# Kernel optimization log

Hardware: AMD Instinct MI355X
Metric: run time of the kernel (lower is better)

Reference implementation:

```python
import jax, jax.numpy as jnp
import numpy as np

B, S, E, H = 4, 4096, 256, 2048
EPS = 1e-5

def layernorm(x, g, b):
    mu = jnp.mean(x, axis=-1, keepdims=True)
    var = jnp.mean(jnp.square(x - mu), axis=-1, keepdims=True)
    return (x - mu) * jax.lax.rsqrt(var + EPS) * g + b

def setup_inputs() -> dict:
    key = jax.random.key(0)
    ks = jax.random.split(key, 16)
    sE = 1.0 / np.sqrt(E)
    sH = 1.0 / np.sqrt(H)
    return {
        "x_embeddings": jax.random.normal(ks[0], (B, S, E), dtype=jnp.float32),
        "wq": jax.random.normal(ks[1], (E, E), dtype=jnp.float32) * sE,
        "bq": jnp.zeros((E,), jnp.float32),
        "wk": jax.random.normal(ks[2], (E, E), dtype=jnp.float32) * sE,
        "bk": jnp.zeros((E,), jnp.float32),
        "wv": jax.random.normal(ks[3], (E, E), dtype=jnp.float32) * sE,
        "bv": jnp.zeros((E,), jnp.float32),
        "w0": jax.random.normal(ks[4], (E, E), dtype=jnp.float32) * sE,
        "b0": jnp.zeros((E,), jnp.float32),
        "w1": jax.random.normal(ks[5], (E, H), dtype=jnp.float32) * sE,
        "b1": jnp.zeros((H,), jnp.float32),
        "ln_mlp_g": jnp.ones((H,), jnp.float32),
        "ln_mlp_b": jnp.zeros((H,), jnp.float32),
        "w2": jax.random.normal(ks[6], (H, E), dtype=jnp.float32) * sH,
        "b2": jnp.zeros((E,), jnp.float32),
        "ln1_g": jnp.ones((E,), jnp.float32),
        "ln1_b": jnp.zeros((E,), jnp.float32),
        "ln2_g": jnp.ones((E,), jnp.float32),
        "ln2_b": jnp.zeros((E,), jnp.float32),
    }

def reference(x_embeddings, wq, bq, wk, bk, wv, bv, w0, b0,
              w1, b1, ln_mlp_g, ln_mlp_b, w2, b2,
              ln1_g, ln1_b, ln2_g, ln2_b):
    x = x_embeddings
    q = x @ wq + bq
    k = x @ wk + bk
    v = x @ wv + bv
    # Unscaled, unmasked attention (faithful to source: no 1/sqrt(d), mask unused)
    scores = jnp.einsum('bqd,bkd->bqk', q, k)          # [B,S,S]
    probs = jax.nn.softmax(scores, axis=-1)
    attn = jnp.einsum('bqk,bkd->bqd', probs, v)        # [B,S,E]
    e = layernorm(x + attn, ln1_g, ln1_b) @ w0 + b0
    h = e @ w1 + b1                                     # [B,S,H]
    h = jax.nn.leaky_relu(layernorm(h, ln_mlp_g, ln_mlp_b))  # LnActivation: LN + LeakyReLU
    logits = h @ w2 + b2                                # [B,S,E]
    return layernorm(jax.nn.leaky_relu(logits + e), ln2_g, ln2_b)
```

## Files before the change

### kernel.cpp

```cpp
#include <hip/hip_runtime.h>

typedef unsigned short u16;
typedef unsigned int   u32;
typedef u16   u16x4 __attribute__((ext_vector_type(4)));
typedef u16   u16x8 __attribute__((ext_vector_type(8)));
typedef short s16x8 __attribute__((ext_vector_type(8)));
typedef float f32x4 __attribute__((ext_vector_type(4)));
typedef _Float16 f16x8 __attribute__((ext_vector_type(8)));

__device__ __forceinline__ u16 f2b(float f) {
  u32 u = __builtin_bit_cast(u32, f);
  u32 r = (u + 0x7fffu + ((u >> 16) & 1u)) >> 16;
  return (u16)r;
}
__device__ __forceinline__ float b2f(u16 h) {
  return __builtin_bit_cast(float, (u32)h << 16);
}
__device__ __forceinline__ u16 f2h(float f) {
  _Float16 h = (_Float16)f;
  return __builtin_bit_cast(u16, h);
}

__device__ __forceinline__ void async16(void* l, const void* g) {
  __builtin_amdgcn_global_load_lds((const __attribute__((address_space(1))) u32*)g,
                                   (__attribute__((address_space(3))) u32*)l, 16, 0, 0);
}

__device__ __forceinline__ float wave_sum(float v) {
#pragma unroll
  for (int m = 32; m; m >>= 1) v += __shfl_xor(v, m, 64);
  return v;
}

constexpr int BM = 128, BN = 128, BK = 64;

template<bool SPLIT, int OMODE>
__global__ __launch_bounds__(256)
void k_gemm_bt(const u16* __restrict__ Ah, const u16* __restrict__ Al, long lda,
               const u16* __restrict__ Bh, const u16* __restrict__ Bl, long ldb,
               const float* __restrict__ bias,
               float* __restrict__ Cf, u16* __restrict__ Cb, u16* __restrict__ Cl,
               long ldc, int K)
{
  __shared__ u16 lds[(SPLIT ? 4 : 2) * BM * BK];
  const int tid = threadIdx.x;
  const long arow0 = (long)blockIdx.y * BM;
  const long bcol0 = (long)blockIdx.x * BN;

  long offA[4], offB[4];
#pragma unroll
  for (int r = 0; r < 4; ++r) {
    const int off = r * 4096 + tid * 16;
    const int row = off >> 7;
    const int colb = off & 127;
    offA[r] = (arow0 + row) * lda + (colb >> 1);
    offB[r] = (bcol0 + row) * ldb + (colb >> 1);
  }

  const int lane = tid & 63;
  const int wid = tid >> 6;
  const int wr = (wid >> 1) * 64;
  const int wc = (wid & 1) * 64;
  const int fr = lane & 15;
  const int fk = (lane >> 4) * 8;

  f32x4 acc[4][4] = {};

  for (int k0 = 0; k0 < K; k0 += BK) {
#pragma unroll
    for (int r = 0; r < 4; ++r) {
      const int loff = (r * 4096 + tid * 16) >> 1;
      async16(&lds[loff],           Ah + offA[r] + k0);
      async16(&lds[BM*BK + loff],   Bh + offB[r] + k0);
      if constexpr (SPLIT) {
        async16(&lds[2*BM*BK + loff], Al + offA[r] + k0);
        async16(&lds[3*BM*BK + loff], Bl + offB[r] + k0);
      }
    }
    __syncthreads();
#pragma unroll
    for (int kk = 0; kk < BK; kk += 32) {
      s16x8 a[4], b[4];
#pragma unroll
      for (int m = 0; m < 4; ++m)
        a[m] = *(const s16x8*)&lds[(wr + m*16 + fr) * BK + kk + fk];
#pragma unroll
      for (int n = 0; n < 4; ++n)
        b[n] = *(const s16x8*)&lds[BM*BK + (wc + n*16 + fr) * BK + kk + fk];
#pragma unroll
      for (int m = 0; m < 4; ++m)
#pragma unroll
        for (int n = 0; n < 4; ++n)
          acc[m][n] = __builtin_amdgcn_mfma_f32_16x16x32_bf16(a[m], b[n], acc[m][n], 0, 0, 0);
      if constexpr (SPLIT) {
        s16x8 al[4], bl[4];
#pragma unroll
        for (int m = 0; m < 4; ++m)
          al[m] = *(const s16x8*)&lds[2*BM*BK + (wr + m*16 + fr) * BK + kk + fk];
#pragma unroll
        for (int n = 0; n < 4; ++n)
          bl[n] = *(const s16x8*)&lds[3*BM*BK + (wc + n*16 + fr) * BK + kk + fk];
#pragma unroll
        for (int m = 0; m < 4; ++m)
#pragma unroll
          for (int n = 0; n < 4; ++n) {
            acc[m][n] = __builtin_amdgcn_mfma_f32_16x16x32_bf16(a[m], bl[n], acc[m][n], 0, 0, 0);
            acc[m][n] = __builtin_amdgcn_mfma_f32_16x16x32_bf16(al[m], b[n], acc[m][n], 0, 0, 0);
          }
      }
    }
    __syncthreads();
  }

  float bv[4];
#pragma unroll
  for (int n = 0; n < 4; ++n) {
    const long gcol = bcol0 + wc + n*16 + fr;
    bv[n] = bias ? bias[gcol] : 0.f;
  }

#pragma unroll
  for (int m = 0; m < 4; ++m) {
#pragma unroll
    for (int reg = 0; reg < 4; ++reg) {
      const long grow = arow0 + wr + m*16 + (lane >> 4) * 4 + reg;
      const long ro = grow * ldc;
#pragma unroll
      for (int n = 0; n < 4; ++n) {
        const long gcol = bcol0 + wc + n*16 + fr;
        const float val = acc[m][n][reg] + bv[n];
        if constexpr (OMODE == 0) {
          Cf[ro + gcol] = val;
        } else if constexpr (OMODE == 1) {
          Cb[ro + gcol] = f2b(val);
        } else if constexpr (OMODE == 4) {
          Cb[ro + gcol] = f2h(val);
        } else {
          const u16 hb = f2b(val);
          Cb[ro + gcol] = hb;
          Cl[ro + gcol] = f2b(val - b2f(hb));
        }
      }
    }
  }
}

__global__ __launch_bounds__(256)
void k_flash(const u16* __restrict__ q16, const u16* __restrict__ k16,
             const u16* __restrict__ vt,
             u16* __restrict__ attn)
{
  __shared__ u16 lkh[2][32*256];
  __shared__ float lS[32*36];
  __shared__ u16 lP[32*40];
  __shared__ float lm[32], ll[32], lsc[32];

  const int tid = threadIdx.x;
  const int lane = tid & 63, wid = tid >> 6;
  const long bo = (long)blockIdx.y * 1048576;
  const long q0 = (long)blockIdx.x * 32;

  const int fr  = lane & 15;
  const int hi2 = lane >> 4;
  const int fk  = hi2 * 8;
  const int qh_sel = wid >> 1;
  const int kh_sel = wid & 1;

  f16x8 qf[8];
  {
    const u16* qp = q16 + bo + (q0 + qh_sel*16 + fr) * 256;
#pragma unroll
    for (int c = 0; c < 8; ++c)
      qf[c] = *(const f16x8*)(qp + c*32 + fk);
  }

  if (tid < 32) { lm[tid] = -1e30f; ll[tid] = 0.f; }
  f32x4 acc[2][4] = {};

  const char* kp = (const char*)(k16 + bo);
  const u16* vbase = vt + bo;

  auto STAGE = [&](int k0s, int b) {
#pragma unroll
    for (int r = 0; r < 4; ++r) {
      const int L = r*4096 + tid*16;
      const int row = L >> 9;
      const int colb = L & 511;
      const long gb = (long)(k0s + row)*512 + (colb ^ ((row & 7) << 4));
      async16((char*)lkh[b] + L, kp + gb);
    }
  };

  STAGE(0, 0);
  __syncthreads();

  int cur = 0;
  for (int k0 = 0; k0 < 4096; k0 += 32) {
    s16x8 vb[4];
#pragma unroll
    for (int j = 0; j < 4; ++j)
      vb[j] = *(const s16x8*)(vbase + (long)(wid*64 + j*16 + fr)*4096 + k0 + fk);

    if (k0 + 32 < 4096) STAGE(k0 + 32, cur ^ 1);

    f32x4 s0 = {};
    const int kc = kh_sel*16 + fr;
    const int swz = (kc & 7) << 4;
#pragma unroll
    for (int c = 0; c < 8; ++c) {
      const int o = (c*64 + hi2*16) ^ swz;
      const f16x8 bh = *(const f16x8*)((const char*)lkh[cur] + kc*512 + o);
      s0 = __builtin_amdgcn_mfma_f32_16x16x32_f16(qf[c], bh, s0, 0, 0, 0);
    }
#pragma unroll
    for (int r = 0; r < 4; ++r)
      lS[(qh_sel*16 + hi2*4 + r)*36 + kh_sel*16 + fr] = s0[r];
    __syncthreads();

    {
      const int sr = tid >> 3;
      const int sc = (tid & 7) * 4;
      const float4 sv = *(const float4*)&lS[sr*36 + sc];
      float tmx = fmaxf(fmaxf(sv.x, sv.y), fmaxf(sv.z, sv.w));
#pragma unroll
      for (int m = 1; m < 8; m <<= 1) tmx = fmaxf(tmx, __shfl_xor(tmx, m, 64));
      const float mold = lm[sr];
      const float mnew = fmaxf(mold, tmx);
      const float p0 = __expf(sv.x - mnew), p1 = __expf(sv.y - mnew);
      const float p2 = __expf(sv.z - mnew), p3 = __expf(sv.w - mnew);
      float ps = p0 + p1 + p2 + p3;
#pragma unroll
      for (int m = 1; m < 8; m <<= 1) ps += __shfl_xor(ps, m, 64);
      const float scale = __expf(mold - mnew);
      if ((tid & 7) == 0) {
        lm[sr] = mnew;
        ll[sr] = ll[sr] * scale + ps;
        lsc[sr] = scale;
      }
      u16x4 pb; pb[0]=f2b(p0); pb[1]=f2b(p1); pb[2]=f2b(p2); pb[3]=f2b(p3);
      *(u16x4*)&lP[sr*40 + sc] = pb;
    }
    __syncthreads();

#pragma unroll
    for (int qm = 0; qm < 2; ++qm)
#pragma unroll
      for (int r = 0; r < 4; ++r) {
        const float s = lsc[qm*16 + hi2*4 + r];
#pragma unroll
        for (int j = 0; j < 4; ++j) acc[qm][j][r] *= s;
      }
#pragma unroll
    for (int qm = 0; qm < 2; ++qm) {
      const s16x8 pa = *(const s16x8*)&lP[(qm*16 + fr)*40 + fk];
#pragma unroll
      for (int j = 0; j < 4; ++j)
        acc[qm][j] = __builtin_amdgcn_mfma_f32_16x16x32_bf16(pa, vb[j], acc[qm][j], 0, 0, 0);
    }
    cur ^= 1;
  }

  __syncthreads();
#pragma unroll
  for (int qm = 0; qm < 2; ++qm)
#pragma unroll
    for (int r = 0; r < 4; ++r) {
      const int row = qm*16 + hi2*4 + r;
      const float inv = 1.0f / ll[row];
      u16* op = attn + bo + (q0 + row)*256 + wid*64 + fr;
#pragma unroll
      for (int j = 0; j < 4; ++j)
        op[j*16] = f2b(acc[qm][j][r] * inv);
    }
}


__global__ __launch_bounds__(256)
void k_split_cast(const float* __restrict__ in, u16* __restrict__ hi, u16* __restrict__ lo, long n4) {
  long i = (long)blockIdx.x * 256 + threadIdx.x;
  if (i >= n4) return;
  float4 v = ((const float4*)in)[i];
  float vv[4] = {v.x, v.y, v.z, v.w};
  u16x4 h, l;
#pragma unroll
  for (int j = 0; j < 4; ++j) {
    u16 hb = f2b(vv[j]);
    h[j] = hb;
    l[j] = f2b(vv[j] - b2f(hb));
  }
  ((u16x4*)hi)[i] = h;
  ((u16x4*)lo)[i] = l;
}

template<bool SPLIT>
__global__ __launch_bounds__(256)
void k_transpose_f32(const float* __restrict__ in, u16* __restrict__ hi, u16* __restrict__ lo,
                     int R, int C) {
  __shared__ float t[32][33];
  const int c0 = blockIdx.x * 32, r0 = blockIdx.y * 32;
  const int tx = threadIdx.x, ty = threadIdx.y;
#pragma unroll
  for (int i = 0; i < 4; ++i)
    t[ty + i*8][tx] = in[(long)(r0 + ty + i*8) * C + c0 + tx];
  __syncthreads();
#pragma unroll
  for (int i = 0; i < 4; ++i) {
    const float f = t[tx][ty + i*8];
    const long o = (long)(c0 + ty + i*8) * R + r0 + tx;
    const u16 hb = f2b(f);
    hi[o] = hb;
    if constexpr (SPLIT) lo[o] = f2b(f - b2f(hb));
  }
}

__global__ __launch_bounds__(256)
void k_transpose_bf16(const u16* __restrict__ in, u16* __restrict__ out,
                      int R, int C, long sIn, long sOut) {
  __shared__ u16 t[32][34];
  const int z = blockIdx.z;
  const u16* ib = in + (long)z * sIn;
  u16* ob = out + (long)z * sOut;
  const int c0 = blockIdx.x * 32, r0 = blockIdx.y * 32;
  const int tx = threadIdx.x, ty = threadIdx.y;
#pragma unroll
  for (int i = 0; i < 4; ++i)
    t[ty + i*8][tx] = ib[(long)(r0 + ty + i*8) * C + c0 + tx];
  __syncthreads();
#pragma unroll
  for (int i = 0; i < 4; ++i)
    ob[(long)(c0 + ty + i*8) * R + r0 + tx] = t[tx][ty + i*8];
}

__global__ __launch_bounds__(256)
void k_add_ln(const float* __restrict__ x, const u16* __restrict__ a,
              const float* __restrict__ g, const float* __restrict__ b,
              u16* __restrict__ out) {
  const long row = (long)blockIdx.x * 4 + (threadIdx.x >> 6);
  const int lane = threadIdx.x & 63;
  const long base = row * 256 + lane * 4;
  const float4 xv = *(const float4*)(x + base);
  const u16x4 av = *(const u16x4*)(a + base);
  float t[4] = {xv.x + b2f(av[0]), xv.y + b2f(av[1]), xv.z + b2f(av[2]), xv.w + b2f(av[3])};
  float s = t[0] + t[1] + t[2] + t[3];
  float q = t[0]*t[0] + t[1]*t[1] + t[2]*t[2] + t[3]*t[3];
  s = wave_sum(s); q = wave_sum(q);
  const float mu = s * (1.f / 256.f);
  const float var = q * (1.f / 256.f) - mu * mu;
  const float rs = rsqrtf(var + 1e-5f);
  const float4 gv = *(const float4*)(g + lane * 4);
  const float4 bv = *(const float4*)(b + lane * 4);
  u16x4 o;
  o[0] = f2b((t[0] - mu) * rs * gv.x + bv.x);
  o[1] = f2b((t[1] - mu) * rs * gv.y + bv.y);
  o[2] = f2b((t[2] - mu) * rs * gv.z + bv.z);
  o[3] = f2b((t[3] - mu) * rs * gv.w + bv.w);
  *(u16x4*)(out + base) = o;
}

__global__ __launch_bounds__(256)
void k_ln_leaky(const u16* __restrict__ h, const float* __restrict__ g,
                const float* __restrict__ b, u16* __restrict__ out) {
  const long row = blockIdx.x;
  const int tid = threadIdx.x;
  const int lane = tid & 63, wid = tid >> 6;
  const u16x8 hv = *(const u16x8*)(h + row * 2048 + tid * 8);
  float f[8];
  float s = 0.f, q = 0.f;
#pragma unroll
  for (int j = 0; j < 8; ++j) { f[j] = b2f(hv[j]); s += f[j]; q += f[j] * f[j]; }
  s = wave_sum(s); q = wave_sum(q);
  __shared__ float rs_[4], rq_[4];
  if (lane == 0) { rs_[wid] = s; rq_[wid] = q; }
  __syncthreads();
  s = rs_[0] + rs_[1] + rs_[2] + rs_[3];
  q = rq_[0] + rq_[1] + rq_[2] + rq_[3];
  const float mu = s * (1.f / 2048.f);
  const float var = q * (1.f / 2048.f) - mu * mu;
  const float rsq = rsqrtf(var + 1e-5f);
  const float4 g0 = *(const float4*)(g + tid * 8);
  const float4 g1 = *(const float4*)(g + tid * 8 + 4);
  const float4 b0 = *(const float4*)(b + tid * 8);
  const float4 b1 = *(const float4*)(b + tid * 8 + 4);
  const float gg[8] = {g0.x, g0.y, g0.z, g0.w, g1.x, g1.y, g1.z, g1.w};
  const float bb[8] = {b0.x, b0.y, b0.z, b0.w, b1.x, b1.y, b1.z, b1.w};
  u16x8 o;
#pragma unroll
  for (int j = 0; j < 8; ++j) {
    float y = (f[j] - mu) * rsq * gg[j] + bb[j];
    y = y > 0.f ? y : 0.01f * y;
    o[j] = f2b(y);
  }
  *(u16x8*)(out + row * 2048 + tid * 8) = o;
}

__global__ __launch_bounds__(256)
void k_final(const float* __restrict__ lg, const u16* __restrict__ e,
             const float* __restrict__ g, const float* __restrict__ b,
             float* __restrict__ out) {
  const long row = (long)blockIdx.x * 4 + (threadIdx.x >> 6);
  const int lane = threadIdx.x & 63;
  const long base = row * 256 + lane * 4;
  const float4 lv = *(const float4*)(lg + base);
  const u16x4 ev = *(const u16x4*)(e + base);
  float t[4] = {lv.x + b2f(ev[0]), lv.y + b2f(ev[1]), lv.z + b2f(ev[2]), lv.w + b2f(ev[3])};
#pragma unroll
  for (int j = 0; j < 4; ++j) t[j] = t[j] > 0.f ? t[j] : 0.01f * t[j];
  float s = t[0] + t[1] + t[2] + t[3];
  float q = t[0]*t[0] + t[1]*t[1] + t[2]*t[2] + t[3]*t[3];
  s = wave_sum(s); q = wave_sum(q);
  const float mu = s * (1.f / 256.f);
  const float var = q * (1.f / 256.f) - mu * mu;
  const float rs = rsqrtf(var + 1e-5f);
  const float4 gv = *(const float4*)(g + lane * 4);
  const float4 bv = *(const float4*)(b + lane * 4);
  float4 o;
  o.x = (t[0] - mu) * rs * gv.x + bv.x;
  o.y = (t[1] - mu) * rs * gv.y + bv.y;
  o.z = (t[2] - mu) * rs * gv.z + bv.z;
  o.w = (t[3] - mu) * rs * gv.w + bv.w;
  *(float4*)(out + base) = o;
}


extern "C" void kernel_launch(void* const* d_in, const int* in_sizes, int n_in,
                              void* d_out, int out_size, void* d_ws, size_t ws_size,
                              hipStream_t stream) {
  const float* x   = (const float*)d_in[0];
  const float* wq  = (const float*)d_in[1];
  const float* bq  = (const float*)d_in[2];
  const float* wk  = (const float*)d_in[3];
  const float* bk  = (const float*)d_in[4];
  const float* wv  = (const float*)d_in[5];
  const float* bv_ = (const float*)d_in[6];
  const float* w0  = (const float*)d_in[7];
  const float* b0  = (const float*)d_in[8];
  const float* w1  = (const float*)d_in[9];
  const float* b1  = (const float*)d_in[10];
  const float* lmg = (const float*)d_in[11];
  const float* lmb = (const float*)d_in[12];
  const float* w2  = (const float*)d_in[13];
  const float* b2  = (const float*)d_in[14];
  const float* l1g = (const float*)d_in[15];
  const float* l1b = (const float*)d_in[16];
  const float* l2g = (const float*)d_in[17];
  const float* l2b = (const float*)d_in[18];

  char* ws = (char*)d_ws;
  float* out = (float*)d_out;

  u16* q16    = (u16*)(ws + 0);
  u16* k16    = (u16*)(ws + 16777216);
  u16* vT     = (u16*)(ws + 33554432);
  u16* x_hi   = (u16*)(ws + 41943040);
  u16* x_lo   = (u16*)(ws + 50331648);
  u16* v_b    = (u16*)(ws + 58720256);
  u16* attn_b = (u16*)(ws + 67108864);
  u16* ln1    = (u16*)(ws + 75497472);
  u16* e_b    = (u16*)(ws + 83886080);
  float* logits = (float*)(ws + 92274688);
  u16* h_b    = (u16*)(ws + 0);
  u16* wqT_h  = (u16*)(ws + 109051904);
  u16* wqT_l  = (u16*)(ws + 109182976);
  u16* wkT_h  = (u16*)(ws + 109314048);
  u16* wkT_l  = (u16*)(ws + 109445120);
  u16* wvT    = (u16*)(ws + 109576192);
  u16* w0T    = (u16*)(ws + 109707264);
  u16* w1T    = (u16*)(ws + 109838336);
  u16* w2T    = (u16*)(ws + 110886912);

  const dim3 t256(256);
  const dim3 tr(32, 8);

  k_split_cast<<<4096, t256, 0, stream>>>(x, x_hi, x_lo, 1048576);
  k_transpose_f32<true ><<<dim3(8, 8),  tr, 0, stream>>>(wq, wqT_h, wqT_l, 256, 256);
  k_transpose_f32<true ><<<dim3(8, 8),  tr, 0, stream>>>(wk, wkT_h, wkT_l, 256, 256);
  k_transpose_f32<false><<<dim3(8, 8),  tr, 0, stream>>>(wv, wvT, nullptr, 256, 256);
  k_transpose_f32<false><<<dim3(8, 8),  tr, 0, stream>>>(w0, w0T, nullptr, 256, 256);
  k_transpose_f32<false><<<dim3(64, 8), tr, 0, stream>>>(w1, w1T, nullptr, 256, 2048);
  k_transpose_f32<false><<<dim3(8, 64), tr, 0, stream>>>(w2, w2T, nullptr, 2048, 256);

  k_gemm_bt<true, 4><<<dim3(2, 128), t256, 0, stream>>>(
      x_hi, x_lo, 256, wqT_h, wqT_l, 256, bq, nullptr, q16, nullptr, 256, 256);
  k_gemm_bt<true, 4><<<dim3(2, 128), t256, 0, stream>>>(
      x_hi, x_lo, 256, wkT_h, wkT_l, 256, bk, nullptr, k16, nullptr, 256, 256);
  k_gemm_bt<false, 1><<<dim3(2, 128), t256, 0, stream>>>(
      x_hi, nullptr, 256, wvT, nullptr, 256, bv_, nullptr, v_b, nullptr, 256, 256);
  k_transpose_bf16<<<dim3(8, 128, 4), tr, 0, stream>>>(v_b, vT, 4096, 256, 1048576, 1048576);

  k_flash<<<dim3(128, 4), t256, 0, stream>>>(q16, k16, vT, attn_b);

  k_add_ln<<<4096, t256, 0, stream>>>(x, attn_b, l1g, l1b, ln1);

  k_gemm_bt<false, 1><<<dim3(2, 128), t256, 0, stream>>>(
      ln1, nullptr, 256, w0T, nullptr, 256, b0, nullptr, e_b, nullptr, 256, 256);
  k_gemm_bt<false, 1><<<dim3(16, 128), t256, 0, stream>>>(
      e_b, nullptr, 256, w1T, nullptr, 256, b1, nullptr, h_b, nullptr, 2048, 256);
  k_ln_leaky<<<16384, t256, 0, stream>>>(h_b, lmg, lmb, h_b);
  k_gemm_bt<false, 0><<<dim3(2, 128), t256, 0, stream>>>(
      h_b, nullptr, 2048, w2T, nullptr, 2048, b2, logits, nullptr, nullptr, 256, 2048);
  k_final<<<4096, t256, 0, stream>>>(logits, e_b, l2g, l2b, out);
}
```

Before: 378.2 us.

## Split flash attention over two key halves and merge partials in add-LN

The flash attention kernel now splits the key dimension into two halves across a new grid axis, doubling the number of blocks and halving each block's serial loop. Each half writes unnormalized bf16 partial outputs plus per-row max and sum statistics. The residual-add LayerNorm kernel merges the two partials with log-sum-exp rescaling before normalizing. This trades extra partial-output traffic and some bf16 rounding of unnormalized accumulators for better GPU occupancy.

```diff
diff --git a/kernel.cpp b/kernel.cpp
--- a/kernel.cpp
+++ b/kernel.cpp
@@ -148,7 +148,8 @@
 __global__ __launch_bounds__(256)
 void k_flash(const u16* __restrict__ q16, const u16* __restrict__ k16,
              const u16* __restrict__ vt,
-             u16* __restrict__ attn)
+             u16* __restrict__ opart,
+             float* __restrict__ stats)
 {
   __shared__ u16 lkh[2][32*256];
   __shared__ float lS[32*36];
@@ -157,8 +158,10 @@
 
   const int tid = threadIdx.x;
   const int lane = tid & 63, wid = tid >> 6;
-  const long bo = (long)blockIdx.y * 1048576;
+  const int khf = blockIdx.y, bz = blockIdx.z;
+  const long bo = (long)bz * 1048576;
   const long q0 = (long)blockIdx.x * 32;
+  const int kbase = khf * 2048;
 
   const int fr  = lane & 15;
   const int hi2 = lane >> 4;
@@ -191,17 +194,19 @@
     }
   };
 
-  STAGE(0, 0);
+  STAGE(kbase, 0);
   __syncthreads();
 
   int cur = 0;
-  for (int k0 = 0; k0 < 4096; k0 += 32) {
+  for (int s = 0; s < 64; ++s) {
+    const int k0 = kbase + s*32;
+
     s16x8 vb[4];
 #pragma unroll
     for (int j = 0; j < 4; ++j)
       vb[j] = *(const s16x8*)(vbase + (long)(wid*64 + j*16 + fr)*4096 + k0 + fk);
 
-    if (k0 + 32 < 4096) STAGE(k0 + 32, cur ^ 1);
+    if (s < 63) STAGE(k0 + 32, cur ^ 1);
 
     f32x4 s0 = {};
     const int kc = kh_sel*16 + fr;
@@ -261,16 +266,21 @@
   }
 
   __syncthreads();
+  if (tid < 32) {
+    const long sb = (long)khf*16384 + (long)bz*4096 + q0 + tid;
+    stats[sb] = lm[tid];
+    stats[32768 + sb] = ll[tid];
+  }
+  u16* ob = opart + (((long)khf*4 + bz)*4096 + q0)*256;
 #pragma unroll
   for (int qm = 0; qm < 2; ++qm)
 #pragma unroll
     for (int r = 0; r < 4; ++r) {
       const int row = qm*16 + hi2*4 + r;
-      const float inv = 1.0f / ll[row];
-      u16* op = attn + bo + (q0 + row)*256 + wid*64 + fr;
+      u16* op = ob + (long)row*256 + wid*64 + fr;
 #pragma unroll
       for (int j = 0; j < 4; ++j)
-        op[j*16] = f2b(acc[qm][j][r] * inv);
+        op[j*16] = f2b(acc[qm][j][r]);
     }
 }
 
@@ -332,20 +342,32 @@
 }
 
 __global__ __launch_bounds__(256)
-void k_add_ln(const float* __restrict__ x, const u16* __restrict__ a,
+void k_add_ln(const float* __restrict__ x, const u16* __restrict__ opart,
+              const float* __restrict__ stats,
               const float* __restrict__ g, const float* __restrict__ b,
               u16* __restrict__ out) {
   const long row = (long)blockIdx.x * 4 + (threadIdx.x >> 6);
   const int lane = threadIdx.x & 63;
+  const long bz = row >> 12, q = row & 4095;
+  const long idx = bz*4096 + q;
+  const float mA = stats[idx],         lA = stats[32768 + idx];
+  const float mB = stats[16384 + idx], lB = stats[32768 + 16384 + idx];
+  const float M = fmaxf(mA, mB);
+  const float ea = __expf(mA - M), eb = __expf(mB - M);
+  const float inv = 1.0f / (ea*lA + eb*lB);
+  const u16x4 OA = *(const u16x4*)(opart + (idx)*256 + lane*4);
+  const u16x4 OB = *(const u16x4*)(opart + (16384 + idx)*256 + lane*4);
   const long base = row * 256 + lane * 4;
   const float4 xv = *(const float4*)(x + base);
-  const u16x4 av = *(const u16x4*)(a + base);
-  float t[4] = {xv.x + b2f(av[0]), xv.y + b2f(av[1]), xv.z + b2f(av[2]), xv.w + b2f(av[3])};
+  float t[4];
+#pragma unroll
+  for (int j = 0; j < 4; ++j)
+    t[j] = ((const float*)&xv)[j] + (ea*b2f(OA[j]) + eb*b2f(OB[j])) * inv;
   float s = t[0] + t[1] + t[2] + t[3];
-  float q = t[0]*t[0] + t[1]*t[1] + t[2]*t[2] + t[3]*t[3];
-  s = wave_sum(s); q = wave_sum(q);
+  float qq = t[0]*t[0] + t[1]*t[1] + t[2]*t[2] + t[3]*t[3];
+  s = wave_sum(s); qq = wave_sum(qq);
   const float mu = s * (1.f / 256.f);
-  const float var = q * (1.f / 256.f) - mu * mu;
+  const float var = qq * (1.f / 256.f) - mu * mu;
   const float rs = rsqrtf(var + 1e-5f);
   const float4 gv = *(const float4*)(g + lane * 4);
   const float4 bv = *(const float4*)(b + lane * 4);
@@ -454,8 +476,8 @@
   u16* x_hi   = (u16*)(ws + 41943040);
   u16* x_lo   = (u16*)(ws + 50331648);
   u16* v_b    = (u16*)(ws + 58720256);
-  u16* attn_b = (u16*)(ws + 67108864);
-  u16* ln1    = (u16*)(ws + 75497472);
+  u16* opart  = (u16*)(ws + 67108864);
+  u16* ln1    = (u16*)(ws + 58720256);
   u16* e_b    = (u16*)(ws + 83886080);
   float* logits = (float*)(ws + 92274688);
   u16* h_b    = (u16*)(ws + 0);
@@ -467,6 +489,7 @@
   u16* w0T    = (u16*)(ws + 109707264);
   u16* w1T    = (u16*)(ws + 109838336);
   u16* w2T    = (u16*)(ws + 110886912);
+  float* stats = (float*)(ws + 111935488);
 
   const dim3 t256(256);
   const dim3 tr(32, 8);
@@ -487,9 +510,9 @@
       x_hi, nullptr, 256, wvT, nullptr, 256, bv_, nullptr, v_b, nullptr, 256, 256);
   k_transpose_bf16<<<dim3(8, 128, 4), tr, 0, stream>>>(v_b, vT, 4096, 256, 1048576, 1048576);
 
-  k_flash<<<dim3(128, 4), t256, 0, stream>>>(q16, k16, vT, attn_b);
-
-  k_add_ln<<<4096, t256, 0, stream>>>(x, attn_b, l1g, l1b, ln1);
+  k_flash<<<dim3(128, 2, 4), t256, 0, stream>>>(q16, k16, vT, opart, stats);
+
+  k_add_ln<<<4096, t256, 0, stream>>>(x, opart, stats, l1g, l1b, ln1);
 
   k_gemm_bt<false, 1><<<dim3(2, 128), t256, 0, stream>>>(
       ln1, nullptr, 256, w0T, nullptr, 256, b0, nullptr, e_b, nullptr, 256, 256);
```

Result: slower. 404.8 us (+7.0%).
